# Kernel tuning notes

Hardware: AMD Instinct MI355X
Metric: run time of the kernel (lower is better)

The kernel has to match this reference:

```python
import jax, jax.numpy as jnp
import numpy as np

B, N, NPOINT, NSAMPLE = 16, 4096, 1024, 32
RADIUS = 0.4
MLP = [64, 64, 128]
IN_CH = 6
EPS = 1e-5


def setup_inputs() -> dict:
    key = jax.random.key(0)
    ks = jax.random.split(key, 2 + 2 * len(MLP))
    inp = {
        "xyz": jax.random.normal(ks[0], (B, 3, N), jnp.float32),
        "points": jax.random.normal(ks[1], (B, 3, N), jnp.float32),
    }
    c_in = IN_CH
    for i, c_out in enumerate(MLP):
        inp[f"W{i}"] = jax.random.normal(ks[2 + 2 * i], (c_out, c_in), jnp.float32) / np.sqrt(c_in).astype(np.float32)
        inp[f"b{i}"] = jnp.zeros((c_out,), jnp.float32)
        inp[f"g{i}"] = jnp.ones((c_out,), jnp.float32)
        inp[f"beta{i}"] = jnp.zeros((c_out,), jnp.float32)
        c_in = c_out
    return inp


def _gather(points, idx):
    # points: [B, N, C], idx: [B, ...] int -> [B, ..., C]
    Bv = points.shape[0]
    flat = idx.reshape(Bv, -1)
    out = jnp.take_along_axis(points, flat[..., None], axis=1)
    return out.reshape(idx.shape + (points.shape[-1],))


def _fps(xyz, npoint):
    # xyz: [B, N, 3] -> centroid indices [B, npoint]
    Bv, Nv, _ = xyz.shape
    bidx = jnp.arange(Bv)

    def step(carry, _):
        dist, far = carry
        cen = xyz[bidx, far][:, None, :]                 # [B,1,3]
        d = jnp.sum((xyz - cen) ** 2, axis=-1)           # [B,N]
        dist = jnp.minimum(dist, d)
        return (dist, jnp.argmax(dist, axis=-1)), far

    init = (jnp.full((Bv, Nv), 1e10, xyz.dtype), jnp.zeros((Bv,), jnp.int32))
    _, cents = jax.lax.scan(step, init, None, length=npoint)
    return jnp.transpose(cents)                          # [B, npoint]


def _square_distance(src, dst):
    # src [B,S,3], dst [B,N,3] -> [B,S,N]
    return (jnp.sum(src ** 2, -1)[:, :, None]
            + jnp.sum(dst ** 2, -1)[:, None, :]
            - 2.0 * jnp.einsum('bsc,bnc->bsn', src, dst))


def _ball_query(radius, nsample, xyz, new_xyz):
    Nv = xyz.shape[1]
    sqr = _square_distance(new_xyz, xyz)                 # [B,S,N]
    arange = jnp.arange(Nv, dtype=jnp.int32)[None, None, :]
    idx = jnp.where(sqr > radius ** 2, Nv, arange)       # invalid -> sentinel N
    idx = jnp.sort(idx, axis=-1)[:, :, :nsample]         # [B,S,K]
    first = idx[:, :, :1]
    return jnp.where(idx == Nv, first, idx)


def reference(xyz, points, W0, b0, g0, beta0, W1, b1, g1, beta1, W2, b2, g2, beta2):
    xyz_t = jnp.transpose(xyz, (0, 2, 1))                # [B,N,3]
    pts_t = jnp.transpose(points, (0, 2, 1))             # [B,N,D]

    fps_idx = _fps(xyz_t, NPOINT)                        # [B,S]
    new_xyz = _gather(xyz_t, fps_idx)                    # [B,S,3]
    idx = _ball_query(RADIUS, NSAMPLE, xyz_t, new_xyz)   # [B,S,K]

    g_xyz = _gather(xyz_t, idx) - new_xyz[:, :, None, :] # [B,S,K,3]
    g_pts = _gather(pts_t, idx)                          # [B,S,K,D]
    feats = jnp.concatenate([g_xyz, g_pts], axis=-1)     # [B,S,K,C]

    for W, b, g, be in ((W0, b0, g0, beta0), (W1, b1, g1, beta1), (W2, b2, g2, beta2)):
        feats = jnp.einsum('bskc,oc->bsko', feats, W) + b
        mean = feats.mean(axis=(0, 1, 2))                # BN train mode stats
        var = feats.var(axis=(0, 1, 2))
        feats = g * (feats - mean) * jax.lax.rsqrt(var + EPS) + be
        feats = jax.nn.relu(feats)

    out = feats.max(axis=2)                              # max over nsample -> [B,S,C]
    return jnp.transpose(new_xyz, (0, 2, 1)), jnp.transpose(out, (0, 2, 1))
```

## Files before the change

kernel.cpp:

```cpp
#include <hip/hip_runtime.h>
#include <hip/hip_bf16.h>

#define B_ 16
#define N_ 4096
#define S_ 1024
#define K_ 32
#define R_ (B_*S_*K_)
#define NBLK_ (R_/64)

typedef unsigned short u16;
typedef __attribute__((ext_vector_type(8))) short bf16x8;
typedef __attribute__((ext_vector_type(4))) float f32x4;

__device__ __forceinline__ u16 f2bf(float f) {
    __hip_bfloat16 h = __float2bfloat16(f);
    return __builtin_bit_cast(u16, h);
}
__device__ __forceinline__ float bf2f(u16 u) {
    unsigned x = ((unsigned)u) << 16;
    return __builtin_bit_cast(float, x);
}

template <int CTRL>
__device__ __forceinline__ double dpp_max_f64(double v) {
    unsigned long long b = (unsigned long long)__double_as_longlong(v);
    int lo = (int)(unsigned)b;
    int hi = (int)(unsigned)(b >> 32);
    int olo = __builtin_amdgcn_update_dpp(lo, lo, CTRL, 0xF, 0xF, false);
    int ohi = __builtin_amdgcn_update_dpp(hi, hi, CTRL, 0xF, 0xF, false);
    double o = __longlong_as_double(
        (long long)(((unsigned long long)(unsigned)ohi << 32) | (unsigned)olo));
    return fmax(v, o);
}

__device__ __forceinline__ double packd(double d, int idx) {
    unsigned long long b = (unsigned long long)__double_as_longlong(d);
    b = (b & ~0xFFFull) | (unsigned)idx;
    return __longlong_as_double((long long)b);
}

__global__ __launch_bounds__(512, 2) void fps_kernel(const float* __restrict__ xyz,
                                                     float* __restrict__ out0) {
    const int b = blockIdx.x;
    const int tid = threadIdx.x;
    const int lane = tid & 63, wid = tid >> 6;
    __shared__ float4 p4[N_];
    __shared__ double candd[2][8];
    const float* xb = xyz + (size_t)b * 3 * N_;

    double x64[8], y64[8], z64[8], q64[8], dist[8];
#pragma unroll
    for (int j = 0; j < 8; ++j) {
        int i = tid + j * 512;
        float x = xb[i], y = xb[N_ + i], z = xb[2 * N_ + i];
        p4[i] = make_float4(x, y, z, 0.f);
        x64[j] = (double)x; y64[j] = (double)y; z64[j] = (double)z;
        q64[j] = x64[j] * x64[j] + y64[j] * y64[j] + z64[j] * z64[j];
        dist[j] = 1e30;
    }
    __syncthreads();

    int far = 0;
    int f0 = 0, f1 = 0;
    for (int s = 0; s < 1023; ++s) {
        float4 c = p4[far];
        f0 = (tid == s) ? far : f0;
        f1 = (tid + 512 == s) ? far : f1;
        double cx = (double)c.x, cy = (double)c.y, cz = (double)c.z;
        double c2p = cx * cx + cy * cy + cz * cz + 1.0;
        double A = -2.0 * cx, Bc = -2.0 * cy, Cc = -2.0 * cz;
#pragma unroll
        for (int j = 0; j < 8; ++j) {
            double d = fma(A, x64[j], fma(Bc, y64[j], fma(Cc, z64[j], q64[j] + c2p)));
            dist[j] = fmin(dist[j], packd(d, tid | (j << 9)));
        }
        double k = fmax(fmax(fmax(dist[0], dist[1]), fmax(dist[2], dist[3])),
                        fmax(fmax(dist[4], dist[5]), fmax(dist[6], dist[7])));
        k = dpp_max_f64<0x111>(k);
        k = dpp_max_f64<0x112>(k);
        k = dpp_max_f64<0x114>(k);
        k = dpp_max_f64<0x118>(k);
        k = dpp_max_f64<0x142>(k);
        k = dpp_max_f64<0x143>(k);
        int buf = s & 1;
        if (lane == 63) candd[buf][wid] = k;
        __syncthreads();
        double k2 = candd[buf][lane & 7];
        k2 = dpp_max_f64<0xB1>(k2);
        k2 = dpp_max_f64<0x4E>(k2);
        k2 = dpp_max_f64<0x124>(k2);
        unsigned lo = (unsigned)(unsigned long long)__double_as_longlong(k2);
        far = (int)(__builtin_amdgcn_readfirstlane(lo) & 0xFFFu);
    }
    if (tid == 511) f1 = far;
    {
        float4 c0 = p4[f0];
        out0[(size_t)b * 3072 + tid]        = c0.x;
        out0[(size_t)b * 3072 + 1024 + tid] = c0.y;
        out0[(size_t)b * 3072 + 2048 + tid] = c0.z;
        float4 c1 = p4[f1];
        out0[(size_t)b * 3072 + 512 + tid]        = c1.x;
        out0[(size_t)b * 3072 + 1024 + 512 + tid] = c1.y;
        out0[(size_t)b * 3072 + 2048 + 512 + tid] = c1.z;
    }
}

__global__ __launch_bounds__(256) void ballq_kernel(const float* __restrict__ xyz,
                                                    const float* __restrict__ out0,
                                                    int* __restrict__ idxbuf) {
    int wid = threadIdx.x >> 6, lane = threadIdx.x & 63;
    int m = blockIdx.x * 4 + wid;
    int b = m >> 10, s = m & 1023;
    const float* xb = xyz + (size_t)b * 3 * N_;
    double cx = (double)out0[b * 3072 + s];
    double cy = (double)out0[b * 3072 + 1024 + s];
    double cz = (double)out0[b * 3072 + 2048 + s];
    double c2 = cx * cx + cy * cy + cz * cz;
    const double rr = 0.4 * 0.4;
    int* ob = idxbuf + (size_t)m * K_;
    int cnt = 0, first = -1;
    for (int ch = 0; ch < N_ / 64; ++ch) {
        int i = ch * 64 + lane;
        double x = (double)xb[i], y = (double)xb[N_ + i], z = (double)xb[2 * N_ + i];
        double p2 = x * x + y * y + z * z;
        double dot = cx * x + cy * y + cz * z;
        double sqr = (c2 + p2) - 2.0 * dot;
        bool in = !(sqr > rr);
        unsigned long long mask = __ballot(in);
        if (in) {
            int pos = cnt + __popcll(mask & ((1ull << lane) - 1ull));
            if (pos < K_) ob[pos] = i;
        }
        if (cnt == 0 && mask) first = ch * 64 + (__ffsll((long long)mask) - 1);
        cnt += __popcll(mask);
        if (cnt >= K_) break;
    }
    if (cnt < K_ && lane >= cnt && lane < K_) ob[lane] = first;
}

__global__ __launch_bounds__(256) void gather_stats0(
        const float* __restrict__ xyz, const float* __restrict__ pts,
        const float* __restrict__ out0, const int* __restrict__ idxbuf,
        const float* __restrict__ W0, const float* __restrict__ b0,
        float* __restrict__ F, float2* __restrict__ part) {
    __shared__ float Fs[64][6];
    __shared__ float W0s[384];
    __shared__ float b0s[64];
    __shared__ float2 red[4][64];
    int tid = threadIdx.x;
    long rowbase = (long)blockIdx.x * 64;
    if (tid < 64) {
        long r = rowbase + tid;
        int b = (int)(r >> 15);
        int rem = (int)(r & 32767);
        int s = rem >> 5;
        int i = idxbuf[r];
        const float* xb = xyz + (size_t)b * 3 * N_;
        const float* pb = pts + (size_t)b * 3 * N_;
        float cx = out0[b * 3072 + s], cy = out0[b * 3072 + 1024 + s], cz = out0[b * 3072 + 2048 + s];
        float f[6];
        f[0] = xb[i] - cx; f[1] = xb[N_ + i] - cy; f[2] = xb[2 * N_ + i] - cz;
        f[3] = pb[i];      f[4] = pb[N_ + i];      f[5] = pb[2 * N_ + i];
        float* Fg = F + (size_t)r * 6;
#pragma unroll
        for (int c = 0; c < 6; ++c) { Fs[tid][c] = f[c]; Fg[c] = f[c]; }
        b0s[tid] = b0[tid];
    }
    for (int t = tid; t < 384; t += 256) W0s[t] = W0[t];
    __syncthreads();
    int o = tid & 63, rg = tid >> 6;
    float w[6];
#pragma unroll
    for (int c = 0; c < 6; ++c) w[c] = W0s[o * 6 + c];
    float sum = 0.f, sq = 0.f;
#pragma unroll
    for (int rr = 0; rr < 16; ++rr) {
        int rl = rg * 16 + rr;
        float y = b0s[o];
#pragma unroll
        for (int c = 0; c < 6; ++c) y += Fs[rl][c] * w[c];
        sum += y; sq += y * y;
    }
    red[rg][o] = make_float2(sum, sq);
    __syncthreads();
    if (tid < 64) {
        float2 t0 = red[0][tid], t1 = red[1][tid], t2 = red[2][tid], t3 = red[3][tid];
        part[(size_t)blockIdx.x * 64 + tid] =
            make_float2(t0.x + t1.x + t2.x + t3.x, t0.y + t1.y + t2.y + t3.y);
    }
}

__global__ __launch_bounds__(256) void reduce_stats(const float2* __restrict__ part,
                                                    int nblk, int C,
                                                    const float* __restrict__ g,
                                                    const float* __restrict__ beta,
                                                    float* __restrict__ scale,
                                                    float* __restrict__ shift) {
    int o = blockIdx.x;
    int tid = threadIdx.x;
    double s = 0.0, q = 0.0;
    for (int i = tid; i < nblk; i += 256) {
        float2 v = part[(size_t)i * C + o];
        s += (double)v.x; q += (double)v.y;
    }
    __shared__ double ss[256], qq[256];
    ss[tid] = s; qq[tid] = q;
    __syncthreads();
    for (int m = 128; m > 0; m >>= 1) {
        if (tid < m) { ss[tid] += ss[tid + m]; qq[tid] += qq[tid + m]; }
        __syncthreads();
    }
    if (tid == 0) {
        const double Rd = (double)R_;
        double mean = ss[0] / Rd;
        double var = qq[0] / Rd - mean * mean;
        double sc = (double)g[o] / sqrt(var + 1e-5);
        scale[o] = (float)sc;
        shift[o] = (float)((double)beta[o] - mean * sc);
    }
}

__global__ __launch_bounds__(256) void cvt_w_kernel(const float* __restrict__ W1,
                                                    const float* __restrict__ W2,
                                                    u16* __restrict__ W1bf,
                                                    u16* __restrict__ W2bf) {
    int t = blockIdx.x * 256 + threadIdx.x;
    if (t < 4096) W1bf[t] = f2bf(W1[t]);
    W2bf[t] = f2bf(W2[t]);
}

__global__ __launch_bounds__(256) void layer1_mfma(
        const float* __restrict__ F, const float* __restrict__ W0,
        const float* __restrict__ b0, const float* __restrict__ scale0,
        const float* __restrict__ shift0, const u16* __restrict__ W1bf,
        const float* __restrict__ b1, u16* __restrict__ Y1bf,
        float2* __restrict__ part) {
    __shared__ float Fs[64][6];
    __shared__ float W0s[384];
    __shared__ float b0s[64], sc0[64], sh0[64];
    __shared__ u16 Xs[64][72];
    __shared__ float ssum[16][64];
    __shared__ float ssq[16][64];
    int tid = threadIdx.x;
    long rowbase = (long)blockIdx.x * 64;
    for (int t = tid; t < 384; t += 256) { Fs[t / 6][t % 6] = F[rowbase * 6 + t]; W0s[t] = W0[t]; }
    if (tid < 64) { b0s[tid] = b0[tid]; sc0[tid] = scale0[tid]; sh0[tid] = shift0[tid]; }
    __syncthreads();
    {
        int o = tid & 63, rg = tid >> 6;
        float w[6];
#pragma unroll
        for (int c = 0; c < 6; ++c) w[c] = W0s[o * 6 + c];
        float sc = sc0[o], sh = sh0[o], bb = b0s[o];
#pragma unroll
        for (int rr = 0; rr < 16; ++rr) {
            int rl = rg * 16 + rr;
            float y = bb;
#pragma unroll
            for (int c = 0; c < 6; ++c) y += Fs[rl][c] * w[c];
            Xs[rl][o] = f2bf(fmaxf(sc * y + sh, 0.f));
        }
    }
    __syncthreads();
    int l = tid & 63, w = tid >> 6;
    int ar = l & 15, kg = l >> 4;
    bf16x8 a0 = *(const bf16x8*)&Xs[w * 16 + ar][kg * 8];
    bf16x8 a1 = *(const bf16x8*)&Xs[w * 16 + ar][32 + kg * 8];
    f32x4 acc[4];
#pragma unroll
    for (int t4 = 0; t4 < 4; ++t4) acc[t4] = (f32x4){0.f, 0.f, 0.f, 0.f};
#pragma unroll
    for (int t4 = 0; t4 < 4; ++t4) {
        const u16* wp = &W1bf[(t4 * 16 + ar) * 64 + kg * 8];
        bf16x8 bfr0 = *(const bf16x8*)wp;
        bf16x8 bfr1 = *(const bf16x8*)(wp + 32);
        acc[t4] = __builtin_amdgcn_mfma_f32_16x16x32_bf16(a0, bfr0, acc[t4], 0, 0, 0);
        acc[t4] = __builtin_amdgcn_mfma_f32_16x16x32_bf16(a1, bfr1, acc[t4], 0, 0, 0);
    }
#pragma unroll
    for (int t4 = 0; t4 < 4; ++t4) {
        int col = t4 * 16 + ar;
        float bb = b1[col];
        float s = 0.f, q = 0.f;
#pragma unroll
        for (int r = 0; r < 4; ++r) {
            float y = acc[t4][r] + bb;
            int row = w * 16 + kg * 4 + r;
            Y1bf[(rowbase + row) * 64 + col] = f2bf(y);
            s += y; q += y * y;
        }
        ssum[w * 4 + kg][col] = s;
        ssq[w * 4 + kg][col] = q;
    }
    __syncthreads();
    if (tid < 64) {
        float s = 0.f, q = 0.f;
#pragma unroll
        for (int i = 0; i < 16; ++i) { s += ssum[i][tid]; q += ssq[i][tid]; }
        part[(size_t)blockIdx.x * 64 + tid] = make_float2(s, q);
    }
}

__global__ __launch_bounds__(256) void layer2_mfma(
        const u16* __restrict__ Y1bf, const float* __restrict__ scale1,
        const float* __restrict__ shift1, const u16* __restrict__ W2bf,
        const float* __restrict__ b2, float* __restrict__ gmax,
        float* __restrict__ gmin, float2* __restrict__ part) {
    __shared__ u16 Xs[64][72];
    __shared__ float sc1s[64], sh1s[64];
    __shared__ float mxs[16][128], mns[16][128];
    __shared__ float ssum[16][128], ssq[16][128];
    int tid = threadIdx.x;
    long rowbase = (long)blockIdx.x * 64;
    if (tid < 64) { sc1s[tid] = scale1[tid]; sh1s[tid] = shift1[tid]; }
    __syncthreads();
    {
        int r = tid >> 2, seg = (tid & 3) * 16;
        const u16* yp = &Y1bf[(rowbase + r) * 64 + seg];
        bf16x8 v0 = *(const bf16x8*)yp;
        bf16x8 v1 = *(const bf16x8*)(yp + 8);
#pragma unroll
        for (int j = 0; j < 8; ++j) {
            float x0 = fmaxf(sc1s[seg + j] * bf2f((u16)v0[j]) + sh1s[seg + j], 0.f);
            float x1 = fmaxf(sc1s[seg + 8 + j] * bf2f((u16)v1[j]) + sh1s[seg + 8 + j], 0.f);
            Xs[r][seg + j] = f2bf(x0);
            Xs[r][seg + 8 + j] = f2bf(x1);
        }
    }
    __syncthreads();
    int l = tid & 63, w = tid >> 6;
    int ar = l & 15, kg = l >> 4;
    bf16x8 a0 = *(const bf16x8*)&Xs[w * 16 + ar][kg * 8];
    bf16x8 a1 = *(const bf16x8*)&Xs[w * 16 + ar][32 + kg * 8];
    f32x4 acc[8];
#pragma unroll
    for (int t8 = 0; t8 < 8; ++t8) acc[t8] = (f32x4){0.f, 0.f, 0.f, 0.f};
#pragma unroll
    for (int t8 = 0; t8 < 8; ++t8) {
        const u16* wp = &W2bf[(t8 * 16 + ar) * 64 + kg * 8];
        bf16x8 bfr0 = *(const bf16x8*)wp;
        bf16x8 bfr1 = *(const bf16x8*)(wp + 32);
        acc[t8] = __builtin_amdgcn_mfma_f32_16x16x32_bf16(a0, bfr0, acc[t8], 0, 0, 0);
        acc[t8] = __builtin_amdgcn_mfma_f32_16x16x32_bf16(a1, bfr1, acc[t8], 0, 0, 0);
    }
#pragma unroll
    for (int t8 = 0; t8 < 8; ++t8) {
        int col = t8 * 16 + ar;
        float bb = b2[col];
        float y0 = acc[t8][0] + bb, y1 = acc[t8][1] + bb;
        float y2 = acc[t8][2] + bb, y3 = acc[t8][3] + bb;
        ssum[w * 4 + kg][col] = y0 + y1 + y2 + y3;
        ssq[w * 4 + kg][col] = y0 * y0 + y1 * y1 + y2 * y2 + y3 * y3;
        mxs[w * 4 + kg][col] = fmaxf(fmaxf(y0, y1), fmaxf(y2, y3));
        mns[w * 4 + kg][col] = fminf(fminf(y0, y1), fminf(y2, y3));
    }
    __syncthreads();
    if (tid < 128) {
        int col = tid;
        float s = 0.f, q = 0.f;
        float m0 = -3.0e38f, m1 = -3.0e38f, n0 = 3.0e38f, n1 = 3.0e38f;
#pragma unroll
        for (int i = 0; i < 8; ++i) {
            s += ssum[i][col]; q += ssq[i][col];
            m0 = fmaxf(m0, mxs[i][col]); n0 = fminf(n0, mns[i][col]);
        }
#pragma unroll
        for (int i = 8; i < 16; ++i) {
            s += ssum[i][col]; q += ssq[i][col];
            m1 = fmaxf(m1, mxs[i][col]); n1 = fminf(n1, mns[i][col]);
        }
        part[(size_t)blockIdx.x * 128 + col] = make_float2(s, q);
        gmax[((size_t)blockIdx.x * 2 + 0) * 128 + col] = m0;
        gmax[((size_t)blockIdx.x * 2 + 1) * 128 + col] = m1;
        gmin[((size_t)blockIdx.x * 2 + 0) * 128 + col] = n0;
        gmin[((size_t)blockIdx.x * 2 + 1) * 128 + col] = n1;
    }
}

__global__ __launch_bounds__(256) void final_kernel(const float* __restrict__ gmax,
                                                    const float* __restrict__ gmin,
                                                    const float* __restrict__ scale2,
                                                    const float* __restrict__ shift2,
                                                    float* __restrict__ out1) {
    int b = blockIdx.x, st = blockIdx.y, ot = blockIdx.z;
    __shared__ float tile[32][33];
    int tid = threadIdx.x;
    for (int e = tid; e < 1024; e += 256) {
        int sl = e >> 5, ol = e & 31;
        int s = st * 32 + sl, o = ot * 32 + ol;
        size_t m = (size_t)b * 1024 + s;
        float sc = scale2[o];
        float v = (sc >= 0.f) ? gmax[m * 128 + o] : gmin[m * 128 + o];
        tile[sl][ol] = fmaxf(sc * v + shift2[o], 0.f);
    }
    __syncthreads();
    for (int e = tid; e < 1024; e += 256) {
        int ol = e >> 5, sl = e & 31;
        int s = st * 32 + sl, o = ot * 32 + ol;
        out1[(size_t)b * 131072 + (size_t)o * 1024 + s] = tile[sl][ol];
    }
}

extern "C" void kernel_launch(void* const* d_in, const int* in_sizes, int n_in,
                              void* d_out, int out_size, void* d_ws, size_t ws_size,
                              hipStream_t stream) {
    const float* xyz   = (const float*)d_in[0];
    const float* pts   = (const float*)d_in[1];
    const float* W0    = (const float*)d_in[2];
    const float* b0    = (const float*)d_in[3];
    const float* g0    = (const float*)d_in[4];
    const float* beta0 = (const float*)d_in[5];
    const float* W1    = (const float*)d_in[6];
    const float* b1    = (const float*)d_in[7];
    const float* g1    = (const float*)d_in[8];
    const float* beta1 = (const float*)d_in[9];
    const float* W2    = (const float*)d_in[10];
    const float* b2    = (const float*)d_in[11];
    const float* g2    = (const float*)d_in[12];
    const float* beta2 = (const float*)d_in[13];

    float* out0 = (float*)d_out;
    float* out1 = (float*)d_out + 49152;

    char* w = (char*)d_ws;
    size_t off = 0;
    int*    idxbuf = (int*)(w + off);    off += (size_t)R_ * 4;
    float*  F      = (float*)(w + off);  off += (size_t)R_ * 6 * 4;
    u16*    Y1bf   = (u16*)(w + off);    off += (size_t)R_ * 64 * 2;
    float*  gmax   = (float*)(w + off);  off += (size_t)B_ * S_ * 128 * 4;
    float*  gmin   = (float*)(w + off);  off += (size_t)B_ * S_ * 128 * 4;
    float2* part   = (float2*)(w + off); off += (size_t)NBLK_ * 128 * 2 * 4;
    u16*    W1bf   = (u16*)(w + off);    off += 4096 * 2;
    u16*    W2bf   = (u16*)(w + off);    off += 8192 * 2;
    float*  ss     = (float*)(w + off);  off += 512 * 4;
    float* scale0 = ss,       *shift0 = ss + 64;
    float* scale1 = ss + 128, *shift1 = ss + 192;
    float* scale2 = ss + 256, *shift2 = ss + 384;

    cvt_w_kernel<<<32, 256, 0, stream>>>(W1, W2, W1bf, W2bf);
    fps_kernel<<<B_, 512, 0, stream>>>(xyz, out0);
    ballq_kernel<<<(B_ * S_) / 4, 256, 0, stream>>>(xyz, out0, idxbuf);
    gather_stats0<<<NBLK_, 256, 0, stream>>>(xyz, pts, out0, idxbuf, W0, b0, F, part);
    reduce_stats<<<64, 256, 0, stream>>>(part, NBLK_, 64, g0, beta0, scale0, shift0);
    layer1_mfma<<<NBLK_, 256, 0, stream>>>(F, W0, b0, scale0, shift0, W1bf, b1, Y1bf, part);
    reduce_stats<<<64, 256, 0, stream>>>(part, NBLK_, 64, g1, beta1, scale1, shift1);
    layer2_mfma<<<NBLK_, 256, 0, stream>>>(Y1bf, scale1, shift1, W2bf, b2, gmax, gmin, part);
    reduce_stats<<<128, 256, 0, stream>>>(part, NBLK_, 128, g2, beta2, scale2, shift2);
    final_kernel<<<dim3(B_, 32, 4), 256, 0, stream>>>(gmax, gmin, scale2, shift2, out1);
}
```

Measured before the change: 857.9 us.

## Recompute layer-1 in layer2, shrink FPS block, precompute double xyz for ball query

```diff
diff --git a/kernel.cpp b/kernel.cpp
--- a/kernel.cpp
+++ b/kernel.cpp
@@ -39,43 +39,52 @@
     return __longlong_as_double((long long)b);
 }
 
-__global__ __launch_bounds__(512, 2) void fps_kernel(const float* __restrict__ xyz,
+__global__ __launch_bounds__(256, 1) void fps_kernel(const float* __restrict__ xyz,
                                                      float* __restrict__ out0) {
     const int b = blockIdx.x;
     const int tid = threadIdx.x;
-    const int lane = tid & 63, wid = tid >> 6;
-    __shared__ float4 p4[N_];
-    __shared__ double candd[2][8];
+    const int lane = tid & 63;
+    __shared__ double xs[N_], ys[N_], zs[N_];
+    __shared__ unsigned long long cand[2];
     const float* xb = xyz + (size_t)b * 3 * N_;
 
-    double x64[8], y64[8], z64[8], q64[8], dist[8];
-#pragma unroll
-    for (int j = 0; j < 8; ++j) {
-        int i = tid + j * 512;
-        float x = xb[i], y = xb[N_ + i], z = xb[2 * N_ + i];
-        p4[i] = make_float4(x, y, z, 0.f);
-        x64[j] = (double)x; y64[j] = (double)y; z64[j] = (double)z;
-        q64[j] = x64[j] * x64[j] + y64[j] * y64[j] + z64[j] * z64[j];
+    double x64[16], y64[16], z64[16], q64[16], dist[16];
+#pragma unroll
+    for (int j = 0; j < 16; ++j) {
+        int i = tid + j * 256;
+        double dx = (double)xb[i], dy = (double)xb[N_ + i], dz = (double)xb[2 * N_ + i];
+        xs[i] = dx; ys[i] = dy; zs[i] = dz;
+        x64[j] = dx; y64[j] = dy; z64[j] = dz;
+        q64[j] = dx * dx + dy * dy + dz * dz;
         dist[j] = 1e30;
     }
+    if (tid < 2) cand[tid] = 0ull;
     __syncthreads();
 
     int far = 0;
-    int f0 = 0, f1 = 0;
+    int f0 = 0, f1 = 0, f2 = 0, f3 = 0;
     for (int s = 0; s < 1023; ++s) {
-        float4 c = p4[far];
-        f0 = (tid == s) ? far : f0;
-        f1 = (tid + 512 == s) ? far : f1;
-        double cx = (double)c.x, cy = (double)c.y, cz = (double)c.z;
+        int sk = s >> 8;
+        int sl = s & 255;
+        if (sk == 0)      f0 = (tid == sl) ? far : f0;
+        else if (sk == 1) f1 = (tid == sl) ? far : f1;
+        else if (sk == 2) f2 = (tid == sl) ? far : f2;
+        else              f3 = (tid == sl) ? far : f3;
+
+        double cx = xs[far], cy = ys[far], cz = zs[far];
         double c2p = cx * cx + cy * cy + cz * cz + 1.0;
         double A = -2.0 * cx, Bc = -2.0 * cy, Cc = -2.0 * cz;
 #pragma unroll
-        for (int j = 0; j < 8; ++j) {
+        for (int j = 0; j < 16; ++j) {
             double d = fma(A, x64[j], fma(Bc, y64[j], fma(Cc, z64[j], q64[j] + c2p)));
-            dist[j] = fmin(dist[j], packd(d, tid | (j << 9)));
-        }
-        double k = fmax(fmax(fmax(dist[0], dist[1]), fmax(dist[2], dist[3])),
-                        fmax(fmax(dist[4], dist[5]), fmax(dist[6], dist[7])));
+            dist[j] = fmin(dist[j], packd(d, tid | (j << 8)));
+        }
+        double m[8];
+#pragma unroll
+        for (int j = 0; j < 8; ++j) m[j] = fmax(dist[2 * j], dist[2 * j + 1]);
+        double m0 = fmax(fmax(m[0], m[1]), fmax(m[2], m[3]));
+        double m1 = fmax(fmax(m[4], m[5]), fmax(m[6], m[7]));
+        double k = fmax(m0, m1);
         k = dpp_max_f64<0x111>(k);
         k = dpp_max_f64<0x112>(k);
         k = dpp_max_f64<0x114>(k);
@@ -83,35 +92,54 @@
         k = dpp_max_f64<0x142>(k);
         k = dpp_max_f64<0x143>(k);
         int buf = s & 1;
-        if (lane == 63) candd[buf][wid] = k;
+        if (lane == 63)
+            atomicMax(&cand[buf], (unsigned long long)__double_as_longlong(k));
+        if (tid == 0) cand[buf ^ 1] = 0ull;
         __syncthreads();
-        double k2 = candd[buf][lane & 7];
-        k2 = dpp_max_f64<0xB1>(k2);
-        k2 = dpp_max_f64<0x4E>(k2);
-        k2 = dpp_max_f64<0x124>(k2);
-        unsigned lo = (unsigned)(unsigned long long)__double_as_longlong(k2);
+        unsigned lo = ((const unsigned*)cand)[buf * 2];
         far = (int)(__builtin_amdgcn_readfirstlane(lo) & 0xFFFu);
     }
-    if (tid == 511) f1 = far;
+    if (tid == 255) f3 = far;
     {
-        float4 c0 = p4[f0];
-        out0[(size_t)b * 3072 + tid]        = c0.x;
-        out0[(size_t)b * 3072 + 1024 + tid] = c0.y;
-        out0[(size_t)b * 3072 + 2048 + tid] = c0.z;
-        float4 c1 = p4[f1];
-        out0[(size_t)b * 3072 + 512 + tid]        = c1.x;
-        out0[(size_t)b * 3072 + 1024 + 512 + tid] = c1.y;
-        out0[(size_t)b * 3072 + 2048 + 512 + tid] = c1.z;
-    }
-}
-
-__global__ __launch_bounds__(256) void ballq_kernel(const float* __restrict__ xyz,
+        float4 w0 = make_float4((float)xs[f0], (float)ys[f0], (float)zs[f0], 0.f);
+        out0[(size_t)b * 3072 + tid]        = w0.x;
+        out0[(size_t)b * 3072 + 1024 + tid] = w0.y;
+        out0[(size_t)b * 3072 + 2048 + tid] = w0.z;
+        out0[(size_t)b * 3072 + 256 + tid]        = (float)xs[f1];
+        out0[(size_t)b * 3072 + 1024 + 256 + tid] = (float)ys[f1];
+        out0[(size_t)b * 3072 + 2048 + 256 + tid] = (float)zs[f1];
+        out0[(size_t)b * 3072 + 512 + tid]        = (float)xs[f2];
+        out0[(size_t)b * 3072 + 1024 + 512 + tid] = (float)ys[f2];
+        out0[(size_t)b * 3072 + 2048 + 512 + tid] = (float)zs[f2];
+        out0[(size_t)b * 3072 + 768 + tid]        = (float)xs[f3];
+        out0[(size_t)b * 3072 + 1024 + 768 + tid] = (float)ys[f3];
+        out0[(size_t)b * 3072 + 2048 + 768 + tid] = (float)zs[f3];
+    }
+}
+
+__global__ __launch_bounds__(256) void prep_kernel(const float* __restrict__ xyz,
+                                                   const float* __restrict__ W1,
+                                                   const float* __restrict__ W2,
+                                                   u16* __restrict__ W1bf,
+                                                   u16* __restrict__ W2bf,
+                                                   double4* __restrict__ xyzq) {
+    int t = blockIdx.x * 256 + threadIdx.x;
+    if (t < 4096) W1bf[t] = f2bf(W1[t]);
+    if (t < 8192) W2bf[t] = f2bf(W2[t]);
+    int b = t >> 12, i = t & 4095;
+    const float* xb = xyz + (size_t)b * 3 * N_;
+    double x = (double)xb[i], y = (double)xb[N_ + i], z = (double)xb[2 * N_ + i];
+    double4 v; v.x = x; v.y = y; v.z = z; v.w = x * x + y * y + z * z;
+    xyzq[t] = v;
+}
+
+__global__ __launch_bounds__(256) void ballq_kernel(const double4* __restrict__ xyzq,
                                                     const float* __restrict__ out0,
                                                     int* __restrict__ idxbuf) {
     int wid = threadIdx.x >> 6, lane = threadIdx.x & 63;
     int m = blockIdx.x * 4 + wid;
     int b = m >> 10, s = m & 1023;
-    const float* xb = xyz + (size_t)b * 3 * N_;
+    const double4* pb = xyzq + (size_t)b * N_;
     double cx = (double)out0[b * 3072 + s];
     double cy = (double)out0[b * 3072 + 1024 + s];
     double cz = (double)out0[b * 3072 + 2048 + s];
@@ -121,10 +149,9 @@
     int cnt = 0, first = -1;
     for (int ch = 0; ch < N_ / 64; ++ch) {
         int i = ch * 64 + lane;
-        double x = (double)xb[i], y = (double)xb[N_ + i], z = (double)xb[2 * N_ + i];
-        double p2 = x * x + y * y + z * z;
-        double dot = cx * x + cy * y + cz * z;
-        double sqr = (c2 + p2) - 2.0 * dot;
+        double4 p = pb[i];
+        double dot = cx * p.x + cy * p.y + cz * p.z;
+        double sqr = (c2 + p.w) - 2.0 * dot;
         bool in = !(sqr > rr);
         unsigned long long mask = __ballot(in);
         if (in) {
@@ -220,21 +247,11 @@
     }
 }
 
-__global__ __launch_bounds__(256) void cvt_w_kernel(const float* __restrict__ W1,
-                                                    const float* __restrict__ W2,
-                                                    u16* __restrict__ W1bf,
-                                                    u16* __restrict__ W2bf) {
-    int t = blockIdx.x * 256 + threadIdx.x;
-    if (t < 4096) W1bf[t] = f2bf(W1[t]);
-    W2bf[t] = f2bf(W2[t]);
-}
-
 __global__ __launch_bounds__(256) void layer1_mfma(
         const float* __restrict__ F, const float* __restrict__ W0,
         const float* __restrict__ b0, const float* __restrict__ scale0,
         const float* __restrict__ shift0, const u16* __restrict__ W1bf,
-        const float* __restrict__ b1, u16* __restrict__ Y1bf,
-        float2* __restrict__ part) {
+        const float* __restrict__ b1, float2* __restrict__ part) {
     __shared__ float Fs[64][6];
     __shared__ float W0s[384];
     __shared__ float b0s[64], sc0[64], sh0[64];
@@ -285,8 +302,6 @@
 #pragma unroll
         for (int r = 0; r < 4; ++r) {
             float y = acc[t4][r] + bb;
-            int row = w * 16 + kg * 4 + r;
-            Y1bf[(rowbase + row) * 64 + col] = f2bf(y);
             s += y; q += y * y;
         }
         ssum[w * 4 + kg][col] = s;
@@ -302,34 +317,72 @@
 }
 
 __global__ __launch_bounds__(256) void layer2_mfma(
-        const u16* __restrict__ Y1bf, const float* __restrict__ scale1,
+        const float* __restrict__ F, const float* __restrict__ W0,
+        const float* __restrict__ b0, const float* __restrict__ scale0,
+        const float* __restrict__ shift0, const u16* __restrict__ W1bf,
+        const float* __restrict__ b1, const float* __restrict__ scale1,
         const float* __restrict__ shift1, const u16* __restrict__ W2bf,
         const float* __restrict__ b2, float* __restrict__ gmax,
         float* __restrict__ gmin, float2* __restrict__ part) {
+    __shared__ float Fs[64][6];
+    __shared__ float W0s[384];
+    __shared__ float b0s[64], sc0[64], sh0[64], b1s[64], sc1s[64], sh1s[64];
     __shared__ u16 Xs[64][72];
-    __shared__ float sc1s[64], sh1s[64];
     __shared__ float mxs[16][128], mns[16][128];
     __shared__ float ssum[16][128], ssq[16][128];
     int tid = threadIdx.x;
     long rowbase = (long)blockIdx.x * 64;
-    if (tid < 64) { sc1s[tid] = scale1[tid]; sh1s[tid] = shift1[tid]; }
+    for (int t = tid; t < 384; t += 256) { Fs[t / 6][t % 6] = F[rowbase * 6 + t]; W0s[t] = W0[t]; }
+    if (tid < 64) {
+        b0s[tid] = b0[tid]; sc0[tid] = scale0[tid]; sh0[tid] = shift0[tid];
+        b1s[tid] = b1[tid]; sc1s[tid] = scale1[tid]; sh1s[tid] = shift1[tid];
+    }
     __syncthreads();
     {
-        int r = tid >> 2, seg = (tid & 3) * 16;
-        const u16* yp = &Y1bf[(rowbase + r) * 64 + seg];
-        bf16x8 v0 = *(const bf16x8*)yp;
-        bf16x8 v1 = *(const bf16x8*)(yp + 8);
-#pragma unroll
-        for (int j = 0; j < 8; ++j) {
-            float x0 = fmaxf(sc1s[seg + j] * bf2f((u16)v0[j]) + sh1s[seg + j], 0.f);
-            float x1 = fmaxf(sc1s[seg + 8 + j] * bf2f((u16)v1[j]) + sh1s[seg + 8 + j], 0.f);
-            Xs[r][seg + j] = f2bf(x0);
-            Xs[r][seg + 8 + j] = f2bf(x1);
+        int o = tid & 63, rg = tid >> 6;
+        float w[6];
+#pragma unroll
+        for (int c = 0; c < 6; ++c) w[c] = W0s[o * 6 + c];
+        float sc = sc0[o], sh = sh0[o], bb = b0s[o];
+#pragma unroll
+        for (int rr = 0; rr < 16; ++rr) {
+            int rl = rg * 16 + rr;
+            float y = bb;
+#pragma unroll
+            for (int c = 0; c < 6; ++c) y += Fs[rl][c] * w[c];
+            Xs[rl][o] = f2bf(fmaxf(sc * y + sh, 0.f));
         }
     }
     __syncthreads();
     int l = tid & 63, w = tid >> 6;
     int ar = l & 15, kg = l >> 4;
+    {
+        bf16x8 a0 = *(const bf16x8*)&Xs[w * 16 + ar][kg * 8];
+        bf16x8 a1 = *(const bf16x8*)&Xs[w * 16 + ar][32 + kg * 8];
+        f32x4 acc1[4];
+#pragma unroll
+        for (int t4 = 0; t4 < 4; ++t4) acc1[t4] = (f32x4){0.f, 0.f, 0.f, 0.f};
+#pragma unroll
+        for (int t4 = 0; t4 < 4; ++t4) {
+            const u16* wp = &W1bf[(t4 * 16 + ar) * 64 + kg * 8];
+            bf16x8 bfr0 = *(const bf16x8*)wp;
+            bf16x8 bfr1 = *(const bf16x8*)(wp + 32);
+            acc1[t4] = __builtin_amdgcn_mfma_f32_16x16x32_bf16(a0, bfr0, acc1[t4], 0, 0, 0);
+            acc1[t4] = __builtin_amdgcn_mfma_f32_16x16x32_bf16(a1, bfr1, acc1[t4], 0, 0, 0);
+        }
+        __syncthreads();
+#pragma unroll
+        for (int t4 = 0; t4 < 4; ++t4) {
+            int col = t4 * 16 + ar;
+            float bb = b1s[col], sc = sc1s[col], sh = sh1s[col];
+#pragma unroll
+            for (int r = 0; r < 4; ++r) {
+                float y = acc1[t4][r] + bb;
+                Xs[w * 16 + kg * 4 + r][col] = f2bf(fmaxf(sc * y + sh, 0.f));
+            }
+        }
+    }
+    __syncthreads();
     bf16x8 a0 = *(const bf16x8*)&Xs[w * 16 + ar][kg * 8];
     bf16x8 a1 = *(const bf16x8*)&Xs[w * 16 + ar][32 + kg * 8];
     f32x4 acc[8];
@@ -424,9 +477,9 @@
 
     char* w = (char*)d_ws;
     size_t off = 0;
+    double4* xyzq = (double4*)(w + off);  off += (size_t)B_ * N_ * 32;
     int*    idxbuf = (int*)(w + off);    off += (size_t)R_ * 4;
     float*  F      = (float*)(w + off);  off += (size_t)R_ * 6 * 4;
-    u16*    Y1bf   = (u16*)(w + off);    off += (size_t)R_ * 64 * 2;
     float*  gmax   = (float*)(w + off);  off += (size_t)B_ * S_ * 128 * 4;
     float*  gmin   = (float*)(w + off);  off += (size_t)B_ * S_ * 128 * 4;
     float2* part   = (float2*)(w + off); off += (size_t)NBLK_ * 128 * 2 * 4;
@@ -437,14 +490,15 @@
     float* scale1 = ss + 128, *shift1 = ss + 192;
     float* scale2 = ss + 256, *shift2 = ss + 384;
 
-    cvt_w_kernel<<<32, 256, 0, stream>>>(W1, W2, W1bf, W2bf);
-    fps_kernel<<<B_, 512, 0, stream>>>(xyz, out0);
-    ballq_kernel<<<(B_ * S_) / 4, 256, 0, stream>>>(xyz, out0, idxbuf);
+    prep_kernel<<<256, 256, 0, stream>>>(xyz, W1, W2, W1bf, W2bf, xyzq);
+    fps_kernel<<<B_, 256, 0, stream>>>(xyz, out0);
+    ballq_kernel<<<(B_ * S_) / 4, 256, 0, stream>>>(xyzq, out0, idxbuf);
     gather_stats0<<<NBLK_, 256, 0, stream>>>(xyz, pts, out0, idxbuf, W0, b0, F, part);
     reduce_stats<<<64, 256, 0, stream>>>(part, NBLK_, 64, g0, beta0, scale0, shift0);
-    layer1_mfma<<<NBLK_, 256, 0, stream>>>(F, W0, b0, scale0, shift0, W1bf, b1, Y1bf, part);
+    layer1_mfma<<<NBLK_, 256, 0, stream>>>(F, W0, b0, scale0, shift0, W1bf, b1, part);
     reduce_stats<<<64, 256, 0, stream>>>(part, NBLK_, 64, g1, beta1, scale1, shift1);
-    layer2_mfma<<<NBLK_, 256, 0, stream>>>(Y1bf, scale1, shift1, W2bf, b2, gmax, gmin, part);
+    layer2_mfma<<<NBLK_, 256, 0, stream>>>(F, W0, b0, scale0, shift0, W1bf, b1,
+                                           scale1, shift1, W2bf, b2, gmax, gmin, part);
     reduce_stats<<<128, 256, 0, stream>>>(part, NBLK_, 128, g2, beta2, scale2, shift2);
     final_kernel<<<dim3(B_, 32, 4), 256, 0, stream>>>(gmax, gmin, scale2, shift2, out1);
 }
```

Measured after the change: 989.0 us. +15.3%, slower.
